# Optimization experiments

Hardware: AMD Instinct MI355X
Metric: run time of the kernel (lower is better)

Reference implementation:

```python
import jax, jax.numpy as jnp
import numpy as np
import math

B, S, H, NH = 2, 4096, 768, 12
HD = H // NH  # 64
LN_EPS = 1e-12


def setup_inputs() -> dict:
    key = jax.random.key(0)
    ks = jax.random.split(key, 6)
    scale = 0.02
    return {
        "hidden_states": jax.random.normal(ks[0], (B, S, H), jnp.float32),
        "attention_mask": jnp.zeros((B, 1, 1, S), jnp.float32),
        "q_w": jax.random.normal(ks[1], (H, H), jnp.float32) * scale,
        "q_b": jnp.zeros((H,), jnp.float32),
        "k_w": jax.random.normal(ks[2], (H, H), jnp.float32) * scale,
        "k_b": jnp.zeros((H,), jnp.float32),
        "v_w": jax.random.normal(ks[3], (H, H), jnp.float32) * scale,
        "v_b": jnp.zeros((H,), jnp.float32),
        "o_w": jax.random.normal(ks[4], (H, H), jnp.float32) * scale,
        "o_b": jnp.zeros((H,), jnp.float32),
        "ln_g": jnp.ones((H,), jnp.float32),
        "ln_b": jnp.zeros((H,), jnp.float32),
    }


def _heads(x):
    # [B,S,H] -> [B,NH,S,HD]
    return x.reshape(B, S, NH, HD).transpose(0, 2, 1, 3)


def reference(hidden_states, attention_mask, q_w, q_b, k_w, k_b, v_w, v_b,
              o_w, o_b, ln_g, ln_b):
    q = _heads(hidden_states @ q_w.T + q_b)
    k = _heads(hidden_states @ k_w.T + k_b)
    v = _heads(hidden_states @ v_w.T + v_b)

    scores = jnp.einsum("bhqd,bhkd->bhqk", q, k) / math.sqrt(HD)
    scores = scores + attention_mask  # additive mask, broadcast [B,1,1,S]
    probs = jax.nn.softmax(scores, axis=-1)  # dropout p=0 in eval
    ctx = jnp.einsum("bhqk,bhkd->bhqd", probs, v)
    ctx = ctx.transpose(0, 2, 1, 3).reshape(B, S, H)

    # Residual block: dense -> (dropout p=0) -> LN(x + input)
    y = ctx @ o_w.T + o_b + hidden_states
    mu = jnp.mean(y, axis=-1, keepdims=True)
    var = jnp.mean(jnp.square(y - mu), axis=-1, keepdims=True)
    out = (y - mu) * jax.lax.rsqrt(var + LN_EPS) * ln_g + ln_b
    return out
```

## Files before the change

kernel.cpp:

```cpp
#include <hip/hip_runtime.h>

typedef __bf16 bf16;
typedef __bf16 bf16x4 __attribute__((ext_vector_type(4)));
typedef __bf16 bf16x8 __attribute__((ext_vector_type(8)));
typedef float f32x4 __attribute__((ext_vector_type(4)));
typedef float f32x16 __attribute__((ext_vector_type(16)));

#define NB 2
#define SEQ 4096
#define HID 768
#define NHEAD 12
#define HDIM 64
#define MTOT (NB * SEQ)
#define LOG2E 1.4426950408889634f

__device__ inline void pack_body(const float* __restrict__ in, bf16* __restrict__ out, int rt) {
    __shared__ alignas(16) bf16 T[16 * 264];
    const int lane = threadIdx.x;
    const int c = lane & 15, g = lane >> 4;
    const float4* in4 = (const float4*)in + (size_t)rt * 16 * (HID / 4);
    for (int chunk = 0; chunk < 3; chunk++) {
#pragma unroll
        for (int i = 0; i < 16; i++) {
            float4 v = in4[(size_t)i * (HID / 4) + chunk * 64 + lane];
            bf16x4 o;
            o[0] = (bf16)v.x; o[1] = (bf16)v.y; o[2] = (bf16)v.z; o[3] = (bf16)v.w;
            *(bf16x4*)&T[i * 264 + lane * 4] = o;
        }
        __syncthreads();
#pragma unroll
        for (int s = 0; s < 8; s++) {
            bf16x8 val = *(const bf16x8*)&T[c * 264 + s * 32 + g * 8];
            *(bf16x8*)(out + (((size_t)rt * 24 + chunk * 8 + s) * 64 + lane) * 8) = val;
        }
        __syncthreads();
    }
}

__global__ __launch_bounds__(64) void pack_a(const float* __restrict__ in, bf16* __restrict__ out) {
    pack_body(in, out, blockIdx.x);
}

__global__ __launch_bounds__(64) void pack_w4(
    const float* __restrict__ w0, const float* __restrict__ w1,
    const float* __restrict__ w2, const float* __restrict__ w3,
    bf16* __restrict__ o0, bf16* __restrict__ o1, bf16* __restrict__ o2, bf16* __restrict__ o3) {
    int y = blockIdx.y;
    const float* in = (y == 0) ? w0 : (y == 1) ? w1 : (y == 2) ? w2 : w3;
    bf16* out = (y == 0) ? o0 : (y == 1) ? o1 : (y == 2) ? o2 : o3;
    pack_body(in, out, blockIdx.x);
}

__global__ __launch_bounds__(256, 2) void qkv_gemm(
    const bf16* __restrict__ Xp,
    const bf16* __restrict__ Wq, const bf16* __restrict__ Wk, const bf16* __restrict__ Wv,
    const float* __restrict__ bq, const float* __restrict__ bk, const float* __restrict__ bv,
    bf16* __restrict__ Qh, bf16* __restrict__ Kh, bf16* __restrict__ Vt)
{
    int z = blockIdx.z;
    const bf16* W = (z == 0) ? Wq : (z == 1) ? Wk : Wv;
    const float* bias = (z == 0) ? bq : (z == 1) ? bk : bv;

    int lane = threadIdx.x & 63;
    int wid  = threadIdx.x >> 6;
    int wm = wid >> 1, wn = wid & 1;
    int g = lane >> 4, c = lane & 15;
    int m0 = blockIdx.y * 128 + wm * 64;
    int n0 = blockIdx.x * 128 + wn * 64;

    f32x4 acc[4][4] = {};
    const bf16* Ap = Xp + ((size_t)(m0 >> 4) * 24) * 512 + (size_t)lane * 8;
    const bf16* Bp = W  + ((size_t)(n0 >> 4) * 24) * 512 + (size_t)lane * 8;

    for (int ks = 0; ks < 24; ks++) {
        bf16x8 a[4], b[4];
#pragma unroll
        for (int i = 0; i < 4; i++) {
            a[i] = *(const bf16x8*)(Ap + ((size_t)i * 24 + ks) * 512);
            b[i] = *(const bf16x8*)(Bp + ((size_t)i * 24 + ks) * 512);
        }
#pragma unroll
        for (int mi = 0; mi < 4; mi++)
#pragma unroll
            for (int ni = 0; ni < 4; ni++)
                acc[mi][ni] = __builtin_amdgcn_mfma_f32_16x16x32_bf16(a[mi], b[ni], acc[mi][ni], 0, 0, 0);
    }

#pragma unroll
    for (int ni = 0; ni < 4; ni++) {
        int n = n0 + ni * 16 + c;
        float bval = bias[n];
        int h = n >> 6, d = n & 63;
#pragma unroll
        for (int mi = 0; mi < 4; mi++) {
#pragma unroll
            for (int j = 0; j < 4; j++) {
                int m = m0 + mi * 16 + g * 4 + j;
                float val = acc[mi][ni][j] + bval;
                int bb = m >> 12, s = m & 4095;
                size_t bhb = (size_t)(bb * NHEAD + h) * SEQ * HDIM;
                if (z == 0) {
                    val *= 0.125f * LOG2E;
                    Qh[bhb + (size_t)s * HDIM + d] = (bf16)val;
                } else if (z == 1) {
                    int fragidx = (((s >> 5) & 1) << 2) | (d >> 4);
                    int lane2 = (s & 31) | (((d >> 3) & 1) << 5);
                    Kh[bhb + (size_t)(s >> 6) * 4096 + fragidx * 512 + lane2 * 8 + (d & 7)] = (bf16)val;
                } else {
                    int fragidx = ((d >> 5) << 2) | ((s >> 4) & 3);
                    int lane2 = (d & 31) | (((s >> 3) & 1) << 5);
                    Vt[bhb + (size_t)(s >> 6) * 4096 + fragidx * 512 + lane2 * 8 + (s & 7)] = (bf16)val;
                }
            }
        }
    }
}

__device__ inline float xhalf_max(float x) {
    float a_ = x, b_ = x;
    asm("v_permlane32_swap_b32 %0, %1" : "+v"(a_), "+v"(b_));
    return fmaxf(a_, b_);
}
__device__ inline float xhalf_sum(float x) {
    float a_ = x, b_ = x;
    asm("v_permlane32_swap_b32 %0, %1" : "+v"(a_), "+v"(b_));
    return a_ + b_;
}

__device__ inline void smax_update(f32x16& sA, f32x16& sB, float& m, float& l,
                                   f32x16& oA, f32x16& oB) {
    float r[16];
#pragma unroll
    for (int i = 0; i < 16; i++) r[i] = fmaxf(sA[i], sB[i]);
#pragma unroll
    for (int st = 8; st; st >>= 1)
#pragma unroll
        for (int i = 0; i < st; i++) r[i] = fmaxf(r[i], r[i + st]);
    float t = xhalf_max(r[0]);
    if (__any(t > m + 8.f)) {
        float mn = fmaxf(m, t);
        float al = __builtin_amdgcn_exp2f(m - mn);
        m = mn; l *= al;
#pragma unroll
        for (int i = 0; i < 16; i++) { oA[i] *= al; oB[i] *= al; }
    }
#pragma unroll
    for (int i = 0; i < 16; i++) {
        sA[i] = __builtin_amdgcn_exp2f(sA[i] - m);
        sB[i] = __builtin_amdgcn_exp2f(sB[i] - m);
    }
    float q[16];
#pragma unroll
    for (int i = 0; i < 16; i++) q[i] = sA[i] + sB[i];
#pragma unroll
    for (int st = 8; st; st >>= 1)
#pragma unroll
        for (int i = 0; i < st; i++) q[i] += q[i + st];
    l += xhalf_sum(q[0]);
}

__device__ inline void pconv(f32x16& sA, f32x16& sB, bf16x8* pa) {
#pragma unroll
    for (int ks = 0; ks < 2; ks++) {
        f32x16& sc = ks ? sB : sA;
        unsigned u[8];
#pragma unroll
        for (int i = 0; i < 8; i++) {
            union { bf16 hh[2]; unsigned uu; } x;
            x.hh[0] = (bf16)sc[i * 2];
            x.hh[1] = (bf16)sc[i * 2 + 1];
            u[i] = x.uu;
        }
        asm("v_permlane32_swap_b32 %0, %1" : "+v"(u[0]), "+v"(u[2]));
        asm("v_permlane32_swap_b32 %0, %1" : "+v"(u[1]), "+v"(u[3]));
        asm("v_permlane32_swap_b32 %0, %1" : "+v"(u[4]), "+v"(u[6]));
        asm("v_permlane32_swap_b32 %0, %1" : "+v"(u[5]), "+v"(u[7]));
        union { unsigned uu[4]; bf16x8 v; } f0, f1;
        f0.uu[0] = u[0]; f0.uu[1] = u[1]; f0.uu[2] = u[2]; f0.uu[3] = u[3];
        f1.uu[0] = u[4]; f1.uu[1] = u[5]; f1.uu[2] = u[6]; f1.uu[3] = u[7];
        pa[ks * 2]     = f0.v;
        pa[ks * 2 + 1] = f1.v;
    }
}

__global__ __launch_bounds__(128, 2) void attn_kernel(
    const bf16* __restrict__ Qh, const bf16* __restrict__ Kh, const bf16* __restrict__ Vt,
    const float* __restrict__ mask, bf16* __restrict__ ctxp)
{
    __shared__ float Sm[4096];
    __shared__ float Sml[256];
    __shared__ alignas(16) bf16 Ep[4096];

    const int lane = threadIdx.x & 63;
    const int w = threadIdx.x >> 6;
    const int lq = lane & 31;
    const int hi = lane >> 5;
    const int bh = blockIdx.x;
    const int b = bh / NHEAD, h = bh % NHEAD;
    const size_t base = (size_t)bh * SEQ * HDIM;
    const int qw = blockIdx.y * 64;

    bf16x8 qf0[4], qf1[4];
#pragma unroll
    for (int dc = 0; dc < 4; dc++) {
        qf0[dc] = *(const bf16x8*)(Qh + base + (size_t)(qw + lq) * HDIM + dc * 16 + hi * 8);
        qf1[dc] = *(const bf16x8*)(Qh + base + (size_t)(qw + 32 + lq) * HDIM + dc * 16 + hi * 8);
    }
    const float* maskb = mask + b * SEQ;

    const bf16* kfrag = Kh + base + (size_t)lane * 8;
    const bf16* vfrag = Vt + base + (size_t)lane * 8;

    float m0 = -3e38f, m1 = -3e38f, l0 = 0.f, l1 = 0.f;
    f32x16 o00 = {}, o01 = {}, o10 = {}, o11 = {};

    for (int kt = w; kt < SEQ / 64; kt += 2) {
        const bf16* kb_ = kfrag + (size_t)kt * 4096;
        const bf16* vb_ = vfrag + (size_t)kt * 4096;
        bf16x8 kv[8];
#pragma unroll
        for (int f = 0; f < 8; f++) kv[f] = *(const bf16x8*)(kb_ + f * 512);

        f32x16 s00 = {}, s01 = {}, s10 = {}, s11 = {};
#pragma unroll
        for (int dc = 0; dc < 4; dc++) {
            s00 = __builtin_amdgcn_mfma_f32_32x32x16_bf16(kv[dc], qf0[dc], s00, 0, 0, 0);
            s10 = __builtin_amdgcn_mfma_f32_32x32x16_bf16(kv[dc], qf1[dc], s10, 0, 0, 0);
        }
#pragma unroll
        for (int dc = 0; dc < 4; dc++) {
            s01 = __builtin_amdgcn_mfma_f32_32x32x16_bf16(kv[4 + dc], qf0[dc], s01, 0, 0, 0);
            s11 = __builtin_amdgcn_mfma_f32_32x32x16_bf16(kv[4 + dc], qf1[dc], s11, 0, 0, 0);
        }

#pragma unroll
        for (int f = 0; f < 8; f++) kv[f] = *(const bf16x8*)(vb_ + f * 512);

        const float* mrow = maskb + kt * 64 + hi * 4;
#pragma unroll
        for (int ks = 0; ks < 2; ks++) {
#pragma unroll
            for (int g = 0; g < 4; g++) {
                f32x4 mk = *(const f32x4*)(mrow + ks * 32 + g * 8);
#pragma unroll
                for (int j = 0; j < 4; j++) {
                    float mval = mk[j] * LOG2E;
                    if (ks == 0) { s00[g * 4 + j] += mval; s10[g * 4 + j] += mval; }
                    else         { s01[g * 4 + j] += mval; s11[g * 4 + j] += mval; }
                }
            }
        }

        bf16x8 pa0[4], pa1[4];
        smax_update(s00, s01, m0, l0, o00, o01);
        pconv(s00, s01, pa0);
        smax_update(s10, s11, m1, l1, o10, o11);
        pconv(s10, s11, pa1);

#pragma unroll
        for (int kc = 0; kc < 4; kc++) {
            o00 = __builtin_amdgcn_mfma_f32_32x32x16_bf16(kv[kc],     pa0[kc], o00, 0, 0, 0);
            o01 = __builtin_amdgcn_mfma_f32_32x32x16_bf16(kv[4 + kc], pa0[kc], o01, 0, 0, 0);
            o10 = __builtin_amdgcn_mfma_f32_32x32x16_bf16(kv[kc],     pa1[kc], o10, 0, 0, 0);
            o11 = __builtin_amdgcn_mfma_f32_32x32x16_bf16(kv[4 + kc], pa1[kc], o11, 0, 0, 0);
        }
    }

    if (w == 1) {
#pragma unroll
        for (int i = 0; i < 16; i++) {
            Sm[i * 64 + lane]        = o00[i];
            Sm[(16 + i) * 64 + lane] = o01[i];
            Sm[(32 + i) * 64 + lane] = o10[i];
            Sm[(48 + i) * 64 + lane] = o11[i];
        }
        Sml[0 * 64 + lane] = m0; Sml[1 * 64 + lane] = l0;
        Sml[2 * 64 + lane] = m1; Sml[3 * 64 + lane] = l1;
    }
    __syncthreads();
    if (w == 1) return;

    {
        float mB0 = Sml[0 * 64 + lane], lB0 = Sml[1 * 64 + lane];
        float mB1 = Sml[2 * 64 + lane], lB1 = Sml[3 * 64 + lane];
        float mm = fmaxf(m0, mB0);
        float a = __builtin_amdgcn_exp2f(m0 - mm);
        float bb_ = __builtin_amdgcn_exp2f(mB0 - mm);
        l0 = l0 * a + lB0 * bb_;
#pragma unroll
        for (int i = 0; i < 16; i++) {
            o00[i] = o00[i] * a + Sm[i * 64 + lane] * bb_;
            o01[i] = o01[i] * a + Sm[(16 + i) * 64 + lane] * bb_;
        }
        mm = fmaxf(m1, mB1);
        a = __builtin_amdgcn_exp2f(m1 - mm);
        bb_ = __builtin_amdgcn_exp2f(mB1 - mm);
        l1 = l1 * a + lB1 * bb_;
#pragma unroll
        for (int i = 0; i < 16; i++) {
            o10[i] = o10[i] * a + Sm[(32 + i) * 64 + lane] * bb_;
            o11[i] = o11[i] * a + Sm[(48 + i) * 64 + lane] * bb_;
        }
    }

    float inv0 = 1.f / l0, inv1 = 1.f / l1;
#pragma unroll
    for (int qh = 0; qh < 2; qh++) {
        f32x16& a = qh ? o10 : o00;
        f32x16& bq_ = qh ? o11 : o01;
        float inv = qh ? inv1 : inv0;
        int q = qh * 32 + lq;
        int sw = (q & 7) << 4;
#pragma unroll
        for (int g = 0; g < 4; g++) {
            bf16x4 p0, p1;
#pragma unroll
            for (int j = 0; j < 4; j++) {
                p0[j] = (bf16)(a[g * 4 + j] * inv);
                p1[j] = (bf16)(bq_[g * 4 + j] * inv);
            }
            int colb = g * 16 + hi * 8;
            *(bf16x4*)((char*)Ep + q * 128 + (colb ^ sw)) = p0;
            *(bf16x4*)((char*)Ep + q * 128 + ((64 + colb) ^ sw)) = p1;
        }
    }
    const int c = lane & 15, g = lane >> 4;
#pragma unroll
    for (int mt = 0; mt < 4; mt++) {
#pragma unroll
        for (int s = 0; s < 2; s++) {
            int row = mt * 16 + c;
            int colb = (s * 64 + g * 16) ^ ((row & 7) << 4);
            bf16x8 val = *(const bf16x8*)((const char*)Ep + row * 128 + colb);
            size_t mtg = (size_t)((b * SEQ + qw) >> 4) + mt;
            *(bf16x8*)(ctxp + ((mtg * 24 + h * 2 + s) * 64 + lane) * 8) = val;
        }
    }
}

__global__ __launch_bounds__(256, 2) void oproj_gemm(
    const bf16* __restrict__ Cp, const bf16* __restrict__ Wo, const float* __restrict__ bo,
    const float* __restrict__ hidden, float* __restrict__ y)
{
    int lane = threadIdx.x & 63;
    int wid  = threadIdx.x >> 6;
    int wm = wid >> 1, wn = wid & 1;
    int g = lane >> 4, c = lane & 15;
    int m0 = blockIdx.y * 128 + wm * 64;
    int n0 = blockIdx.x * 128 + wn * 64;

    f32x4 acc[4][4] = {};
    const bf16* Ap = Cp + ((size_t)(m0 >> 4) * 24) * 512 + (size_t)lane * 8;
    const bf16* Bp = Wo + ((size_t)(n0 >> 4) * 24) * 512 + (size_t)lane * 8;

    for (int ks = 0; ks < 24; ks++) {
        bf16x8 a[4], b[4];
#pragma unroll
        for (int i = 0; i < 4; i++) {
            a[i] = *(const bf16x8*)(Ap + ((size_t)i * 24 + ks) * 512);
            b[i] = *(const bf16x8*)(Bp + ((size_t)i * 24 + ks) * 512);
        }
#pragma unroll
        for (int mi = 0; mi < 4; mi++)
#pragma unroll
            for (int ni = 0; ni < 4; ni++)
                acc[mi][ni] = __builtin_amdgcn_mfma_f32_16x16x32_bf16(a[mi], b[ni], acc[mi][ni], 0, 0, 0);
    }

#pragma unroll
    for (int ni = 0; ni < 4; ni++) {
        int n = n0 + ni * 16 + c;
        float bval = bo[n];
#pragma unroll
        for (int mi = 0; mi < 4; mi++) {
#pragma unroll
            for (int j = 0; j < 4; j++) {
                int m = m0 + mi * 16 + g * 4 + j;
                size_t idx = (size_t)m * HID + n;
                y[idx] = acc[mi][ni][j] + bval + hidden[idx];
            }
        }
    }
}

__global__ __launch_bounds__(256) void ln_kernel(
    const float* __restrict__ y, const float* __restrict__ gam,
    const float* __restrict__ bet, float* __restrict__ out)
{
    int row = blockIdx.x * 4 + (threadIdx.x >> 6);
    int lane = threadIdx.x & 63;
    const float* yr = y + (size_t)row * HID;

    float4 v[3];
#pragma unroll
    for (int i = 0; i < 3; i++)
        v[i] = reinterpret_cast<const float4*>(yr)[lane + i * 64];

    float s = 0.f;
#pragma unroll
    for (int i = 0; i < 3; i++) s += v[i].x + v[i].y + v[i].z + v[i].w;
#pragma unroll
    for (int msk = 1; msk < 64; msk <<= 1) s += __shfl_xor(s, msk, 64);
    float mean = s * (1.f / 768.f);

    float q = 0.f;
#pragma unroll
    for (int i = 0; i < 3; i++) {
        float dx = v[i].x - mean, dy = v[i].y - mean, dz = v[i].z - mean, dw = v[i].w - mean;
        q += dx * dx + dy * dy + dz * dz + dw * dw;
    }
#pragma unroll
    for (int msk = 1; msk < 64; msk <<= 1) q += __shfl_xor(q, msk, 64);
    float rstd = rsqrtf(q * (1.f / 768.f) + 1e-12f);

    float* outr = out + (size_t)row * HID;
#pragma unroll
    for (int i = 0; i < 3; i++) {
        float4 gg = reinterpret_cast<const float4*>(gam)[lane + i * 64];
        float4 bb = reinterpret_cast<const float4*>(bet)[lane + i * 64];
        float4 o;
        o.x = (v[i].x - mean) * rstd * gg.x + bb.x;
        o.y = (v[i].y - mean) * rstd * gg.y + bb.y;
        o.z = (v[i].z - mean) * rstd * gg.z + bb.z;
        o.w = (v[i].w - mean) * rstd * gg.w + bb.w;
        reinterpret_cast<float4*>(outr)[lane + i * 64] = o;
    }
}

extern "C" void kernel_launch(void* const* d_in, const int* in_sizes, int n_in,
                              void* d_out, int out_size, void* d_ws, size_t ws_size,
                              hipStream_t stream) {
    const float* hidden = (const float*)d_in[0];
    const float* mask   = (const float*)d_in[1];
    const float* q_w = (const float*)d_in[2];
    const float* q_b = (const float*)d_in[3];
    const float* k_w = (const float*)d_in[4];
    const float* k_b = (const float*)d_in[5];
    const float* v_w = (const float*)d_in[6];
    const float* v_b = (const float*)d_in[7];
    const float* o_w = (const float*)d_in[8];
    const float* o_b = (const float*)d_in[9];
    const float* ln_g = (const float*)d_in[10];
    const float* ln_b = (const float*)d_in[11];
    float* out = (float*)d_out;

    const size_t SZ_X = (size_t)MTOT * HID;
    const size_t SZ_W = (size_t)HID * HID;

    char* ws = (char*)d_ws;
    size_t XB_OFF = 0;
    size_t W_OFF  = XB_OFF + SZ_X * 2;
    size_t QH_OFF = W_OFF + 4 * SZ_W * 2;
    size_t KH_OFF = QH_OFF + SZ_X * 2;
    size_t VT_OFF = KH_OFF + SZ_X * 2;

    bf16* Xp  = (bf16*)(ws + XB_OFF);
    bf16* Wqp = (bf16*)(ws + W_OFF);
    bf16* Wkp = Wqp + SZ_W;
    bf16* Wvp = Wkp + SZ_W;
    bf16* Wop = Wvp + SZ_W;
    bf16* Qh  = (bf16*)(ws + QH_OFF);
    bf16* Kh  = (bf16*)(ws + KH_OFF);
    bf16* Vt  = (bf16*)(ws + VT_OFF);
    bf16* ctxp = (bf16*)(ws + XB_OFF);
    float* y  = (float*)(ws + QH_OFF);

    pack_a<<<dim3(MTOT / 16), 64, 0, stream>>>(hidden, Xp);
    pack_w4<<<dim3(HID / 16, 4), 64, 0, stream>>>(q_w, k_w, v_w, o_w, Wqp, Wkp, Wvp, Wop);

    qkv_gemm<<<dim3(HID / 128, MTOT / 128, 3), 256, 0, stream>>>(
        Xp, Wqp, Wkp, Wvp, q_b, k_b, v_b, Qh, Kh, Vt);

    attn_kernel<<<dim3(NB * NHEAD, SEQ / 64), 128, 0, stream>>>(Qh, Kh, Vt, mask, ctxp);

    oproj_gemm<<<dim3(HID / 128, MTOT / 128), 256, 0, stream>>>(ctxp, Wop, o_b, hidden, y);

    ln_kernel<<<dim3(MTOT / 4), 256, 0, stream>>>(y, ln_g, ln_b, out);
}
```

Baseline: 297.6 us.

## Split attention work into four waves with 32-query, 32-key tiles per wave

The attention block grows from 2 to 4 waves. Each wave now handles 32 queries and processes 32-key half-tiles, interleaved with its partner wave, instead of 64 queries by 64-key tiles. Per-wave register pressure drops (one S accumulator and two O accumulators instead of four each), so launch bounds can allow 4 blocks per SM and raise occupancy for latency hiding. The cost is more MFMA issue overhead per unit of work, narrower per-wave loads, and K/V fragments being read by two query-group waves instead of reused inside one.

```diff
diff --git a/kernel.cpp b/kernel.cpp
--- a/kernel.cpp
+++ b/kernel.cpp
@@ -127,13 +127,12 @@
     return a_ + b_;
 }
 
-__device__ inline void smax_update(f32x16& sA, f32x16& sB, float& m, float& l,
-                                   f32x16& oA, f32x16& oB) {
-    float r[16];
-#pragma unroll
-    for (int i = 0; i < 16; i++) r[i] = fmaxf(sA[i], sB[i]);
-#pragma unroll
-    for (int st = 8; st; st >>= 1)
+__device__ inline void smax16(f32x16& s, float& m, float& l, f32x16& o0, f32x16& o1) {
+    float r[8];
+#pragma unroll
+    for (int i = 0; i < 8; i++) r[i] = fmaxf(s[i], s[i + 8]);
+#pragma unroll
+    for (int st = 4; st; st >>= 1)
 #pragma unroll
         for (int i = 0; i < st; i++) r[i] = fmaxf(r[i], r[i + st]);
     float t = xhalf_max(r[0]);
@@ -142,198 +141,160 @@
         float al = __builtin_amdgcn_exp2f(m - mn);
         m = mn; l *= al;
 #pragma unroll
-        for (int i = 0; i < 16; i++) { oA[i] *= al; oB[i] *= al; }
-    }
-#pragma unroll
-    for (int i = 0; i < 16; i++) {
-        sA[i] = __builtin_amdgcn_exp2f(sA[i] - m);
-        sB[i] = __builtin_amdgcn_exp2f(sB[i] - m);
-    }
-    float q[16];
-#pragma unroll
-    for (int i = 0; i < 16; i++) q[i] = sA[i] + sB[i];
-#pragma unroll
-    for (int st = 8; st; st >>= 1)
+        for (int i = 0; i < 16; i++) { o0[i] *= al; o1[i] *= al; }
+    }
+#pragma unroll
+    for (int i = 0; i < 16; i++) s[i] = __builtin_amdgcn_exp2f(s[i] - m);
+    float q[8];
+#pragma unroll
+    for (int i = 0; i < 8; i++) q[i] = s[i] + s[i + 8];
+#pragma unroll
+    for (int st = 4; st; st >>= 1)
 #pragma unroll
         for (int i = 0; i < st; i++) q[i] += q[i + st];
     l += xhalf_sum(q[0]);
 }
 
-__device__ inline void pconv(f32x16& sA, f32x16& sB, bf16x8* pa) {
-#pragma unroll
-    for (int ks = 0; ks < 2; ks++) {
-        f32x16& sc = ks ? sB : sA;
-        unsigned u[8];
-#pragma unroll
-        for (int i = 0; i < 8; i++) {
-            union { bf16 hh[2]; unsigned uu; } x;
-            x.hh[0] = (bf16)sc[i * 2];
-            x.hh[1] = (bf16)sc[i * 2 + 1];
-            u[i] = x.uu;
-        }
-        asm("v_permlane32_swap_b32 %0, %1" : "+v"(u[0]), "+v"(u[2]));
-        asm("v_permlane32_swap_b32 %0, %1" : "+v"(u[1]), "+v"(u[3]));
-        asm("v_permlane32_swap_b32 %0, %1" : "+v"(u[4]), "+v"(u[6]));
-        asm("v_permlane32_swap_b32 %0, %1" : "+v"(u[5]), "+v"(u[7]));
-        union { unsigned uu[4]; bf16x8 v; } f0, f1;
-        f0.uu[0] = u[0]; f0.uu[1] = u[1]; f0.uu[2] = u[2]; f0.uu[3] = u[3];
-        f1.uu[0] = u[4]; f1.uu[1] = u[5]; f1.uu[2] = u[6]; f1.uu[3] = u[7];
-        pa[ks * 2]     = f0.v;
-        pa[ks * 2 + 1] = f1.v;
-    }
-}
-
-__global__ __launch_bounds__(128, 2) void attn_kernel(
+__device__ inline void pconv16(const f32x16& sc, bf16x8* pa) {
+    unsigned u[8];
+#pragma unroll
+    for (int i = 0; i < 8; i++) {
+        union { bf16 hh[2]; unsigned uu; } x;
+        x.hh[0] = (bf16)sc[i * 2];
+        x.hh[1] = (bf16)sc[i * 2 + 1];
+        u[i] = x.uu;
+    }
+    asm("v_permlane32_swap_b32 %0, %1" : "+v"(u[0]), "+v"(u[2]));
+    asm("v_permlane32_swap_b32 %0, %1" : "+v"(u[1]), "+v"(u[3]));
+    asm("v_permlane32_swap_b32 %0, %1" : "+v"(u[4]), "+v"(u[6]));
+    asm("v_permlane32_swap_b32 %0, %1" : "+v"(u[5]), "+v"(u[7]));
+    union { unsigned uu[4]; bf16x8 v; } f0, f1;
+    f0.uu[0] = u[0]; f0.uu[1] = u[1]; f0.uu[2] = u[2]; f0.uu[3] = u[3];
+    f1.uu[0] = u[4]; f1.uu[1] = u[5]; f1.uu[2] = u[6]; f1.uu[3] = u[7];
+    pa[0] = f0.v;
+    pa[1] = f1.v;
+}
+
+__global__ __launch_bounds__(256, 4) void attn_kernel(
     const bf16* __restrict__ Qh, const bf16* __restrict__ Kh, const bf16* __restrict__ Vt,
     const float* __restrict__ mask, bf16* __restrict__ ctxp)
 {
-    __shared__ float Sm[4096];
-    __shared__ float Sml[256];
-    __shared__ alignas(16) bf16 Ep[4096];
+    __shared__ float Sm[2][2048];
+    __shared__ float Sml[2][128];
+    __shared__ alignas(16) bf16 Ep[2][2048];
 
     const int lane = threadIdx.x & 63;
-    const int w = threadIdx.x >> 6;
+    const int wid = threadIdx.x >> 6;
+    const int qg = wid >> 1;
+    const int kp = wid & 1;
     const int lq = lane & 31;
     const int hi = lane >> 5;
     const int bh = blockIdx.x;
     const int b = bh / NHEAD, h = bh % NHEAD;
     const size_t base = (size_t)bh * SEQ * HDIM;
-    const int qw = blockIdx.y * 64;
-
-    bf16x8 qf0[4], qf1[4];
-#pragma unroll
-    for (int dc = 0; dc < 4; dc++) {
-        qf0[dc] = *(const bf16x8*)(Qh + base + (size_t)(qw + lq) * HDIM + dc * 16 + hi * 8);
-        qf1[dc] = *(const bf16x8*)(Qh + base + (size_t)(qw + 32 + lq) * HDIM + dc * 16 + hi * 8);
-    }
+    const int qw = blockIdx.y * 64 + qg * 32;
+
+    bf16x8 qf[4];
+#pragma unroll
+    for (int dc = 0; dc < 4; dc++)
+        qf[dc] = *(const bf16x8*)(Qh + base + (size_t)(qw + lq) * HDIM + dc * 16 + hi * 8);
+
     const float* maskb = mask + b * SEQ;
-
     const bf16* kfrag = Kh + base + (size_t)lane * 8;
     const bf16* vfrag = Vt + base + (size_t)lane * 8;
 
-    float m0 = -3e38f, m1 = -3e38f, l0 = 0.f, l1 = 0.f;
-    f32x16 o00 = {}, o01 = {}, o10 = {}, o11 = {};
-
-    for (int kt = w; kt < SEQ / 64; kt += 2) {
-        const bf16* kb_ = kfrag + (size_t)kt * 4096;
-        const bf16* vb_ = vfrag + (size_t)kt * 4096;
-        bf16x8 kv[8];
-#pragma unroll
-        for (int f = 0; f < 8; f++) kv[f] = *(const bf16x8*)(kb_ + f * 512);
-
-        f32x16 s00 = {}, s01 = {}, s10 = {}, s11 = {};
-#pragma unroll
-        for (int dc = 0; dc < 4; dc++) {
-            s00 = __builtin_amdgcn_mfma_f32_32x32x16_bf16(kv[dc], qf0[dc], s00, 0, 0, 0);
-            s10 = __builtin_amdgcn_mfma_f32_32x32x16_bf16(kv[dc], qf1[dc], s10, 0, 0, 0);
-        }
-#pragma unroll
-        for (int dc = 0; dc < 4; dc++) {
-            s01 = __builtin_amdgcn_mfma_f32_32x32x16_bf16(kv[4 + dc], qf0[dc], s01, 0, 0, 0);
-            s11 = __builtin_amdgcn_mfma_f32_32x32x16_bf16(kv[4 + dc], qf1[dc], s11, 0, 0, 0);
-        }
-
-#pragma unroll
-        for (int f = 0; f < 8; f++) kv[f] = *(const bf16x8*)(vb_ + f * 512);
-
-        const float* mrow = maskb + kt * 64 + hi * 4;
-#pragma unroll
-        for (int ks = 0; ks < 2; ks++) {
-#pragma unroll
-            for (int g = 0; g < 4; g++) {
-                f32x4 mk = *(const f32x4*)(mrow + ks * 32 + g * 8);
-#pragma unroll
-                for (int j = 0; j < 4; j++) {
-                    float mval = mk[j] * LOG2E;
-                    if (ks == 0) { s00[g * 4 + j] += mval; s10[g * 4 + j] += mval; }
-                    else         { s01[g * 4 + j] += mval; s11[g * 4 + j] += mval; }
-                }
-            }
-        }
-
-        bf16x8 pa0[4], pa1[4];
-        smax_update(s00, s01, m0, l0, o00, o01);
-        pconv(s00, s01, pa0);
-        smax_update(s10, s11, m1, l1, o10, o11);
-        pconv(s10, s11, pa1);
-
-#pragma unroll
-        for (int kc = 0; kc < 4; kc++) {
-            o00 = __builtin_amdgcn_mfma_f32_32x32x16_bf16(kv[kc],     pa0[kc], o00, 0, 0, 0);
-            o01 = __builtin_amdgcn_mfma_f32_32x32x16_bf16(kv[4 + kc], pa0[kc], o01, 0, 0, 0);
-            o10 = __builtin_amdgcn_mfma_f32_32x32x16_bf16(kv[kc],     pa1[kc], o10, 0, 0, 0);
-            o11 = __builtin_amdgcn_mfma_f32_32x32x16_bf16(kv[4 + kc], pa1[kc], o11, 0, 0, 0);
-        }
-    }
-
-    if (w == 1) {
+    float m = -3e38f, l = 0.f;
+    f32x16 o0 = {}, o1 = {};
+
+    for (int t = 0; t < SEQ / 64; t++) {
+        const int kt = 2 * t + kp;
+        const size_t tb = (size_t)(kt >> 1) * 4096;
+        const int khalf = kt & 1;
+
+        bf16x8 kf[4];
+#pragma unroll
+        for (int dc = 0; dc < 4; dc++)
+            kf[dc] = *(const bf16x8*)(kfrag + tb + (khalf * 4 + dc) * 512);
+
+        f32x16 s = {};
+#pragma unroll
+        for (int dc = 0; dc < 4; dc++)
+            s = __builtin_amdgcn_mfma_f32_32x32x16_bf16(kf[dc], qf[dc], s, 0, 0, 0);
+
+        bf16x8 vf[4];
+        vf[0] = *(const bf16x8*)(vfrag + tb + (khalf * 2 + 0) * 512);
+        vf[1] = *(const bf16x8*)(vfrag + tb + (khalf * 2 + 1) * 512);
+        vf[2] = *(const bf16x8*)(vfrag + tb + (4 + khalf * 2 + 0) * 512);
+        vf[3] = *(const bf16x8*)(vfrag + tb + (4 + khalf * 2 + 1) * 512);
+
+        const float* mrow = maskb + kt * 32 + hi * 4;
+#pragma unroll
+        for (int g = 0; g < 4; g++) {
+            f32x4 mk = *(const f32x4*)(mrow + g * 8);
+#pragma unroll
+            for (int j = 0; j < 4; j++)
+                s[g * 4 + j] += mk[j] * LOG2E;
+        }
+
+        smax16(s, m, l, o0, o1);
+        bf16x8 pa[2];
+        pconv16(s, pa);
+
+        o0 = __builtin_amdgcn_mfma_f32_32x32x16_bf16(vf[0], pa[0], o0, 0, 0, 0);
+        o0 = __builtin_amdgcn_mfma_f32_32x32x16_bf16(vf[1], pa[1], o0, 0, 0, 0);
+        o1 = __builtin_amdgcn_mfma_f32_32x32x16_bf16(vf[2], pa[0], o1, 0, 0, 0);
+        o1 = __builtin_amdgcn_mfma_f32_32x32x16_bf16(vf[3], pa[1], o1, 0, 0, 0);
+    }
+
+    if (kp == 1) {
 #pragma unroll
         for (int i = 0; i < 16; i++) {
-            Sm[i * 64 + lane]        = o00[i];
-            Sm[(16 + i) * 64 + lane] = o01[i];
-            Sm[(32 + i) * 64 + lane] = o10[i];
-            Sm[(48 + i) * 64 + lane] = o11[i];
-        }
-        Sml[0 * 64 + lane] = m0; Sml[1 * 64 + lane] = l0;
-        Sml[2 * 64 + lane] = m1; Sml[3 * 64 + lane] = l1;
+            Sm[qg][i * 64 + lane]        = o0[i];
+            Sm[qg][(16 + i) * 64 + lane] = o1[i];
+        }
+        Sml[qg][lane] = m; Sml[qg][64 + lane] = l;
     }
     __syncthreads();
-    if (w == 1) return;
+    if (kp == 1) return;
 
     {
-        float mB0 = Sml[0 * 64 + lane], lB0 = Sml[1 * 64 + lane];
-        float mB1 = Sml[2 * 64 + lane], lB1 = Sml[3 * 64 + lane];
-        float mm = fmaxf(m0, mB0);
-        float a = __builtin_amdgcn_exp2f(m0 - mm);
-        float bb_ = __builtin_amdgcn_exp2f(mB0 - mm);
-        l0 = l0 * a + lB0 * bb_;
+        float mB = Sml[qg][lane], lB = Sml[qg][64 + lane];
+        float mm = fmaxf(m, mB);
+        float a = __builtin_amdgcn_exp2f(m - mm);
+        float bb_ = __builtin_amdgcn_exp2f(mB - mm);
+        l = l * a + lB * bb_;
 #pragma unroll
         for (int i = 0; i < 16; i++) {
-            o00[i] = o00[i] * a + Sm[i * 64 + lane] * bb_;
-            o01[i] = o01[i] * a + Sm[(16 + i) * 64 + lane] * bb_;
-        }
-        mm = fmaxf(m1, mB1);
-        a = __builtin_amdgcn_exp2f(m1 - mm);
-        bb_ = __builtin_amdgcn_exp2f(mB1 - mm);
-        l1 = l1 * a + lB1 * bb_;
-#pragma unroll
-        for (int i = 0; i < 16; i++) {
-            o10[i] = o10[i] * a + Sm[(32 + i) * 64 + lane] * bb_;
-            o11[i] = o11[i] * a + Sm[(48 + i) * 64 + lane] * bb_;
-        }
-    }
-
-    float inv0 = 1.f / l0, inv1 = 1.f / l1;
-#pragma unroll
-    for (int qh = 0; qh < 2; qh++) {
-        f32x16& a = qh ? o10 : o00;
-        f32x16& bq_ = qh ? o11 : o01;
-        float inv = qh ? inv1 : inv0;
-        int q = qh * 32 + lq;
-        int sw = (q & 7) << 4;
-#pragma unroll
-        for (int g = 0; g < 4; g++) {
-            bf16x4 p0, p1;
-#pragma unroll
-            for (int j = 0; j < 4; j++) {
-                p0[j] = (bf16)(a[g * 4 + j] * inv);
-                p1[j] = (bf16)(bq_[g * 4 + j] * inv);
-            }
-            int colb = g * 16 + hi * 8;
-            *(bf16x4*)((char*)Ep + q * 128 + (colb ^ sw)) = p0;
-            *(bf16x4*)((char*)Ep + q * 128 + ((64 + colb) ^ sw)) = p1;
-        }
-    }
-    const int c = lane & 15, g = lane >> 4;
-#pragma unroll
-    for (int mt = 0; mt < 4; mt++) {
-#pragma unroll
-        for (int s = 0; s < 2; s++) {
+            o0[i] = o0[i] * a + Sm[qg][i * 64 + lane] * bb_;
+            o1[i] = o1[i] * a + Sm[qg][(16 + i) * 64 + lane] * bb_;
+        }
+    }
+
+    float inv = 1.f / l;
+    bf16* ep = Ep[qg];
+    const int sw = (lq & 7) << 4;
+#pragma unroll
+    for (int g = 0; g < 4; g++) {
+        bf16x4 p0, p1;
+#pragma unroll
+        for (int j = 0; j < 4; j++) {
+            p0[j] = (bf16)(o0[g * 4 + j] * inv);
+            p1[j] = (bf16)(o1[g * 4 + j] * inv);
+        }
+        int colb = g * 16 + hi * 8;
+        *(bf16x4*)((char*)ep + lq * 128 + (colb ^ sw)) = p0;
+        *(bf16x4*)((char*)ep + lq * 128 + ((64 + colb) ^ sw)) = p1;
+    }
+    const int c = lane & 15, gg = lane >> 4;
+#pragma unroll
+    for (int mt = 0; mt < 2; mt++) {
+#pragma unroll
+        for (int s2 = 0; s2 < 2; s2++) {
             int row = mt * 16 + c;
-            int colb = (s * 64 + g * 16) ^ ((row & 7) << 4);
-            bf16x8 val = *(const bf16x8*)((const char*)Ep + row * 128 + colb);
+            int colb = (s2 * 64 + gg * 16) ^ ((row & 7) << 4);
+            bf16x8 val = *(const bf16x8*)((const char*)ep + row * 128 + colb);
             size_t mtg = (size_t)((b * SEQ + qw) >> 4) + mt;
-            *(bf16x8*)(ctxp + ((mtg * 24 + h * 2 + s) * 64 + lane) * 8) = val;
+            *(bf16x8*)(ctxp + ((mtg * 24 + h * 2 + s2) * 64 + lane) * 8) = val;
         }
     }
 }
@@ -471,7 +432,7 @@
     qkv_gemm<<<dim3(HID / 128, MTOT / 128, 3), 256, 0, stream>>>(
         Xp, Wqp, Wkp, Wvp, q_b, k_b, v_b, Qh, Kh, Vt);
 
-    attn_kernel<<<dim3(NB * NHEAD, SEQ / 64), 128, 0, stream>>>(Qh, Kh, Vt, mask, ctxp);
+    attn_kernel<<<dim3(NB * NHEAD, SEQ / 64), 256, 0, stream>>>(Qh, Kh, Vt, mask, ctxp);
 
     oproj_gemm<<<dim3(HID / 128, MTOT / 128), 256, 0, stream>>>(ctxp, Wop, o_b, hidden, y);
 
```

Result: faster. 273.4 us (-8.1%).
